# Optimization experiments

Hardware: AMD Instinct MI355X
Metric: run time of the kernel (lower is better)

## Reference

```python
import jax, jax.numpy as jnp
import numpy as np

D_MODEL = 1024
N_HEADS = 16
N_SPECIAL = 4
N_STD = N_HEADS - N_SPECIAL
D_K = D_MODEL // N_HEADS


def setup_inputs() -> dict:
    key = jax.random.key(0)
    ks = jax.random.split(key, 8)
    B, S = 2, 2048
    x = jax.random.normal(ks[0], (B, S, D_MODEL), dtype=jnp.float32)
    input_ids = jax.random.randint(ks[1], (B, S), 0, 32000)
    w = lambda k: jax.random.normal(k, (D_MODEL, D_MODEL), dtype=jnp.float32) * 0.02
    return {
        "x": x,
        "input_ids": input_ids,
        "Wq": w(ks[2]), "bq": jnp.zeros((D_MODEL,), jnp.float32),
        "Wk": w(ks[3]), "bk": jnp.zeros((D_MODEL,), jnp.float32),
        "Wv": w(ks[4]), "bv": jnp.zeros((D_MODEL,), jnp.float32),
        "Wo": w(ks[5]), "bo": jnp.zeros((D_MODEL,), jnp.float32),
    }


def _sdpa(q, k, v):
    # q,k,v: [B, H, S, Dk]
    scale = 1.0 / jnp.sqrt(jnp.float32(D_K))
    scores = jnp.einsum("bhqd,bhkd->bhqk", q, k) * scale
    weights = jax.nn.softmax(scores, axis=-1)
    out = jnp.einsum("bhqk,bhkd->bhqd", weights, v)
    return out, weights


def reference(x, input_ids, Wq, bq, Wk, bk, Wv, bv, Wo, bo):
    B, S, _ = x.shape
    split = lambda t: jnp.transpose(t.reshape(B, S, N_HEADS, D_K), (0, 2, 1, 3))
    q = split(x @ Wq + bq)  # [B, H, S, Dk]
    k = split(x @ Wk + bk)
    v = split(x @ Wv + bv)
    # split head groups: first N_STD standard heads, last N_SPECIAL special heads
    std_out, std_w = _sdpa(q[:, :N_STD], k[:, :N_STD], v[:, :N_STD])
    spec_out, spec_w = _sdpa(q[:, N_STD:], k[:, N_STD:], v[:, N_STD:])
    out = jnp.concatenate([std_out, spec_out], axis=1)  # [B, H, S, Dk]
    out = jnp.transpose(out, (0, 2, 1, 3)).reshape(B, S, D_MODEL)
    out = out @ Wo + bo
    return out, std_w, spec_w
```

## Files before the change

### kernel.cpp

```cpp
#include <hip/hip_runtime.h>
#include <hip/hip_bf16.h>
#include <stdint.h>

#define S_LEN 2048
#define DM    1024
#define NHEAD 16
#define DKH   64

typedef __attribute__((ext_vector_type(8))) short short8;
typedef __attribute__((ext_vector_type(4))) float floatx4;

__device__ __forceinline__ unsigned short f2b(float f) {
  union { float f; unsigned u; } v; v.f = f;
  unsigned u = v.u;
  u += 0x7FFF + ((u >> 16) & 1);
  return (unsigned short)(u >> 16);
}

__global__ void cast_x_kernel(const float* __restrict__ x, unsigned short* __restrict__ xb) {
  int i = (blockIdx.x * 256 + threadIdx.x) * 4;
  float4 v = *(const float4*)(x + i);
  uint2 p;
  p.x = (unsigned)f2b(v.x) | ((unsigned)f2b(v.y) << 16);
  p.y = (unsigned)f2b(v.z) | ((unsigned)f2b(v.w) << 16);
  *(uint2*)(xb + i) = p;
}

__global__ void castT_w_kernel(const float* __restrict__ Wq, const float* __restrict__ Wk,
                               const float* __restrict__ Wv, const float* __restrict__ Wo,
                               unsigned short* __restrict__ Wqt, unsigned short* __restrict__ Wkt,
                               unsigned short* __restrict__ Wvt, unsigned short* __restrict__ Wot) {
  __shared__ __align__(16) unsigned short tile[64][68];
  int z = blockIdx.z;
  const float* W = (z == 0) ? Wq : (z == 1) ? Wk : (z == 2) ? Wv : Wo;
  unsigned short* O = (z == 0) ? Wqt : (z == 1) ? Wkt : (z == 2) ? Wvt : Wot;
  int kbase = blockIdx.y * 64, nbase = blockIdx.x * 64;
  int t = threadIdx.x;
  int r = t >> 4, c = (t & 15) * 4;
#pragma unroll
  for (int i = 0; i < 4; ++i) {
    int row = r + i * 16;
    float4 v = *(const float4*)(W + (size_t)(kbase + row) * DM + nbase + c);
    tile[row][c]     = f2b(v.x); tile[row][c + 1] = f2b(v.y);
    tile[row][c + 2] = f2b(v.z); tile[row][c + 3] = f2b(v.w);
  }
  __syncthreads();
  int n0 = t >> 4, k0 = (t & 15) * 4;
#pragma unroll
  for (int i = 0; i < 4; ++i) {
    int n = n0 + i * 16;
    uint2 p;
    p.x = (unsigned)tile[k0][n]     | ((unsigned)tile[k0 + 1][n] << 16);
    p.y = (unsigned)tile[k0 + 2][n] | ((unsigned)tile[k0 + 3][n] << 16);
    *(uint2*)(O + (size_t)(nbase + n) * DM + kbase + k0) = p;
  }
}

__global__ __launch_bounds__(256) void gemm_kernel(
    const unsigned short* __restrict__ A,
    const unsigned short* __restrict__ Wt0, const unsigned short* __restrict__ Wt1,
    const unsigned short* __restrict__ Wt2,
    const float* __restrict__ b0, const float* __restrict__ b1, const float* __restrict__ b2,
    unsigned short* __restrict__ o0, unsigned short* __restrict__ o1,
    unsigned short* __restrict__ o2, float* __restrict__ o3, int qkv) {
  __shared__ __align__(16) unsigned short sA[128][40];
  __shared__ __align__(16) unsigned short sB[128][40];
  int z = blockIdx.z;
  const unsigned short* Wt = (!qkv || z == 0) ? Wt0 : (z == 1) ? Wt1 : Wt2;
  const float* bias        = (!qkv || z == 0) ? b0  : (z == 1) ? b1  : b2;
  int bm = blockIdx.y, bn = blockIdx.x;
  int t = threadIdx.x;
  int w = t >> 6, lane = t & 63, lm = lane & 15, q4 = lane >> 4;
  int wm = w >> 1, wn = w & 1;
  floatx4 acc[4][4];
#pragma unroll
  for (int i = 0; i < 4; ++i)
#pragma unroll
    for (int j = 0; j < 4; ++j) acc[i][j] = (floatx4){0.f, 0.f, 0.f, 0.f};

  for (int kk = 0; kk < 32; ++kk) {
    __syncthreads();
#pragma unroll
    for (int i = 0; i < 2; ++i) {
      int u = t + 256 * i;
      int row = u >> 2, seg = u & 3;
      *(uint4*)&sA[row][seg * 8] = *(const uint4*)(A + (size_t)(bm * 128 + row) * DM + kk * 32 + seg * 8);
      *(uint4*)&sB[row][seg * 8] = *(const uint4*)(Wt + (size_t)(bn * 128 + row) * DM + kk * 32 + seg * 8);
    }
    __syncthreads();
    short8 af[4], bf[4];
#pragma unroll
    for (int tm = 0; tm < 4; ++tm) af[tm] = *(const short8*)&sA[wm * 64 + tm * 16 + lm][q4 * 8];
#pragma unroll
    for (int tn = 0; tn < 4; ++tn) bf[tn] = *(const short8*)&sB[wn * 64 + tn * 16 + lm][q4 * 8];
#pragma unroll
    for (int tm = 0; tm < 4; ++tm)
#pragma unroll
      for (int tn = 0; tn < 4; ++tn)
        acc[tm][tn] = __builtin_amdgcn_mfma_f32_16x16x32_bf16(af[tm], bf[tn], acc[tm][tn], 0, 0, 0);
  }

  const float qscale = 0.18033688011112042f;
#pragma unroll
  for (int tm = 0; tm < 4; ++tm) {
    int mrow = bm * 128 + wm * 64 + tm * 16 + q4 * 4;
#pragma unroll
    for (int tn = 0; tn < 4; ++tn) {
      int n = bn * 128 + wn * 64 + tn * 16 + lm;
      float bv = bias[n];
#pragma unroll
      for (int r = 0; r < 4; ++r) {
        int m = mrow + r;
        float val = acc[tm][tn][r] + bv;
        if (qkv) {
          int b = m >> 11, s = m & 2047, h = n >> 6, d = n & 63;
          unsigned short* op = (z == 0) ? o0 : (z == 1) ? o1 : o2;
          op[(size_t)((b * NHEAD + h) * S_LEN + s) * DKH + d] = f2b(z == 0 ? val * qscale : val);
        } else {
          o3[(size_t)m * DM + n] = val;
        }
      }
    }
  }
}

__global__ void transpose_v_kernel(const unsigned short* __restrict__ V, unsigned short* __restrict__ Vt) {
  __shared__ __align__(16) unsigned short tile[64][72];
  int b = blockIdx.z, h = blockIdx.y, st = blockIdx.x;
  size_t head = (size_t)(b * NHEAD + h) * S_LEN * DKH;
  int t = threadIdx.x;
#pragma unroll
  for (int i = 0; i < 2; ++i) {
    int u = t + 256 * i;
    int row = u >> 3, seg = u & 7;
    *(uint4*)&tile[row][seg * 8] = *(const uint4*)(V + head + (size_t)(st * 64 + row) * DKH + seg * 8);
  }
  __syncthreads();
#pragma unroll
  for (int i = 0; i < 2; ++i) {
    int u = t + 256 * i;
    int d = u >> 3, sg = u & 7;
    unsigned short vals[8];
#pragma unroll
    for (int j = 0; j < 8; ++j) vals[j] = tile[sg * 8 + j][d];
    uint4 p;
    p.x = (unsigned)vals[0] | ((unsigned)vals[1] << 16);
    p.y = (unsigned)vals[2] | ((unsigned)vals[3] << 16);
    p.z = (unsigned)vals[4] | ((unsigned)vals[5] << 16);
    p.w = (unsigned)vals[6] | ((unsigned)vals[7] << 16);
    *(uint4*)(Vt + head + (size_t)d * S_LEN + st * 64 + sg * 8) = p;
  }
}

__global__ __launch_bounds__(256) void attn_kernel(
    const unsigned short* __restrict__ Q, const unsigned short* __restrict__ K,
    const unsigned short* __restrict__ Vt, float* __restrict__ wout,
    unsigned short* __restrict__ ctx) {
  __shared__ __align__(16) unsigned short sQ[64][72];
  __shared__ __align__(16) unsigned short sK[64][72];
  __shared__ __align__(16) unsigned short sV[64][72];
  __shared__ __align__(16) unsigned short sP[64][72];
  int qt = blockIdx.x, h = blockIdx.y, b = blockIdx.z;
  size_t head = (size_t)(b * NHEAD + h) * S_LEN * DKH;
  int q0 = qt * 64;
  int t = threadIdx.x, w = t >> 6, lane = t & 63, lm = lane & 15, q4 = lane >> 4;
#pragma unroll
  for (int i = 0; i < 2; ++i) {
    int u = t + 256 * i;
    int row = u >> 3, seg = u & 7;
    *(uint4*)&sQ[row][seg * 8] = *(const uint4*)(Q + head + (size_t)(q0 + row) * DKH + seg * 8);
  }
  __syncthreads();
  short8 qf0 = *(const short8*)&sQ[w * 16 + lm][q4 * 8];
  short8 qf1 = *(const short8*)&sQ[w * 16 + lm][32 + q4 * 8];

  float lsum[4] = {0.f, 0.f, 0.f, 0.f};
  for (int c = 0; c < 32; ++c) {
    __syncthreads();
#pragma unroll
    for (int i = 0; i < 2; ++i) {
      int u = t + 256 * i;
      int row = u >> 3, seg = u & 7;
      *(uint4*)&sK[row][seg * 8] = *(const uint4*)(K + head + (size_t)(c * 64 + row) * DKH + seg * 8);
    }
    __syncthreads();
#pragma unroll
    for (int s4 = 0; s4 < 4; ++s4) {
      short8 kf0 = *(const short8*)&sK[s4 * 16 + lm][q4 * 8];
      short8 kf1 = *(const short8*)&sK[s4 * 16 + lm][32 + q4 * 8];
      floatx4 zz = (floatx4){0.f, 0.f, 0.f, 0.f};
      zz = __builtin_amdgcn_mfma_f32_16x16x32_bf16(qf0, kf0, zz, 0, 0, 0);
      zz = __builtin_amdgcn_mfma_f32_16x16x32_bf16(qf1, kf1, zz, 0, 0, 0);
#pragma unroll
      for (int r = 0; r < 4; ++r) lsum[r] += exp2f(zz[r]);
    }
  }
#pragma unroll
  for (int off = 1; off < 16; off <<= 1)
#pragma unroll
    for (int r = 0; r < 4; ++r) lsum[r] += __shfl_xor(lsum[r], off, 64);
  float rl[4];
#pragma unroll
  for (int r = 0; r < 4; ++r) rl[r] = 1.0f / lsum[r];

  size_t wbase = (h < 12) ? (4194304ULL + (size_t)(b * 12 + h) * 4194304ULL)
                          : (104857600ULL + (size_t)(b * 4 + h - 12) * 4194304ULL);

  floatx4 acc[4];
#pragma unroll
  for (int i = 0; i < 4; ++i) acc[i] = (floatx4){0.f, 0.f, 0.f, 0.f};
  for (int c = 0; c < 32; ++c) {
    __syncthreads();
#pragma unroll
    for (int i = 0; i < 2; ++i) {
      int u = t + 256 * i;
      int row = u >> 3, seg = u & 7;
      *(uint4*)&sK[row][seg * 8] = *(const uint4*)(K + head + (size_t)(c * 64 + row) * DKH + seg * 8);
      *(uint4*)&sV[row][seg * 8] = *(const uint4*)(Vt + head + (size_t)row * S_LEN + c * 64 + seg * 8);
    }
    __syncthreads();
#pragma unroll
    for (int s4 = 0; s4 < 4; ++s4) {
      short8 kf0 = *(const short8*)&sK[s4 * 16 + lm][q4 * 8];
      short8 kf1 = *(const short8*)&sK[s4 * 16 + lm][32 + q4 * 8];
      floatx4 zz = (floatx4){0.f, 0.f, 0.f, 0.f};
      zz = __builtin_amdgcn_mfma_f32_16x16x32_bf16(qf0, kf0, zz, 0, 0, 0);
      zz = __builtin_amdgcn_mfma_f32_16x16x32_bf16(qf1, kf1, zz, 0, 0, 0);
#pragma unroll
      for (int r = 0; r < 4; ++r) {
        float p = exp2f(zz[r]) * rl[r];
        wout[wbase + (size_t)(q0 + w * 16 + q4 * 4 + r) * S_LEN + c * 64 + s4 * 16 + lm] = p;
        sP[w * 16 + q4 * 4 + r][s4 * 16 + lm] = f2b(p);
      }
    }
    __syncthreads();
#pragma unroll
    for (int ks = 0; ks < 2; ++ks) {
      short8 pa = *(const short8*)&sP[w * 16 + lm][ks * 32 + q4 * 8];
#pragma unroll
      for (int nt = 0; nt < 4; ++nt) {
        short8 vb = *(const short8*)&sV[nt * 16 + lm][ks * 32 + q4 * 8];
        acc[nt] = __builtin_amdgcn_mfma_f32_16x16x32_bf16(pa, vb, acc[nt], 0, 0, 0);
      }
    }
  }
#pragma unroll
  for (int nt = 0; nt < 4; ++nt)
#pragma unroll
    for (int r = 0; r < 4; ++r)
      ctx[(size_t)(b * S_LEN + q0 + w * 16 + q4 * 4 + r) * DM + h * DKH + nt * 16 + lm] = f2b(acc[nt][r]);
}

extern "C" void kernel_launch(void* const* d_in, const int* in_sizes, int n_in,
                              void* d_out, int out_size, void* d_ws, size_t ws_size,
                              hipStream_t stream) {
  const float* x  = (const float*)d_in[0];
  const float* Wq = (const float*)d_in[2];
  const float* bq = (const float*)d_in[3];
  const float* Wk = (const float*)d_in[4];
  const float* bk = (const float*)d_in[5];
  const float* Wv = (const float*)d_in[6];
  const float* bv = (const float*)d_in[7];
  const float* Wo = (const float*)d_in[8];
  const float* bo = (const float*)d_in[9];
  float* out = (float*)d_out;

  char* ws = (char*)d_ws;
  unsigned short* xb  = (unsigned short*)(ws + 0);
  unsigned short* Wqt = (unsigned short*)(ws + 8388608);
  unsigned short* Wkt = (unsigned short*)(ws + 10485760);
  unsigned short* Wvt = (unsigned short*)(ws + 12582912);
  unsigned short* Wot = (unsigned short*)(ws + 14680064);
  unsigned short* Qb  = (unsigned short*)(ws + 16777216);
  unsigned short* Kb  = (unsigned short*)(ws + 25165824);
  unsigned short* Vb  = (unsigned short*)(ws + 33554432);
  unsigned short* Vtb = (unsigned short*)(ws + 41943040);
  unsigned short* ctx = (unsigned short*)(ws + 50331648);

  cast_x_kernel<<<4096, 256, 0, stream>>>(x, xb);
  castT_w_kernel<<<dim3(16, 16, 4), 256, 0, stream>>>(Wq, Wk, Wv, Wo, Wqt, Wkt, Wvt, Wot);
  gemm_kernel<<<dim3(8, 32, 3), 256, 0, stream>>>(xb, Wqt, Wkt, Wvt, bq, bk, bv,
                                                  Qb, Kb, Vb, nullptr, 1);
  transpose_v_kernel<<<dim3(32, NHEAD, 2), 256, 0, stream>>>(Vb, Vtb);
  attn_kernel<<<dim3(32, NHEAD, 2), 256, 0, stream>>>(Qb, Kb, Vtb, out, ctx);
  gemm_kernel<<<dim3(8, 32, 1), 256, 0, stream>>>(ctx, Wot, nullptr, nullptr, bo, nullptr, nullptr,
                                                  nullptr, nullptr, nullptr, out, 0);
}
```

Before: 816.4 us.

## Transpose QK^T MFMA operands for row-contiguous vectorized weight stores

The K and Q operands of the score MFMA are swapped, so each lane holds four consecutive key columns of a single query row instead of four rows. This makes the row-sum reduction a scalar with two cross-lane shuffles, and lets the fp32 attention-weight output be written as one 16-byte nontemporal store per lane instead of four scattered scalar stores. The bf16 probabilities are packed with a hardware cvt_pk instruction and written to shared memory as one 8-byte store. The main target is the large weights write, which dominates memory traffic. Because the bf16 conversion now uses hardware rounding instead of the software routine, numerics may differ slightly.

```diff
diff --git a/kernel.cpp b/kernel.cpp
--- a/kernel.cpp
+++ b/kernel.cpp
@@ -174,7 +174,7 @@
   short8 qf0 = *(const short8*)&sQ[w * 16 + lm][q4 * 8];
   short8 qf1 = *(const short8*)&sQ[w * 16 + lm][32 + q4 * 8];
 
-  float lsum[4] = {0.f, 0.f, 0.f, 0.f};
+  float lsum = 0.f;
   for (int c = 0; c < 32; ++c) {
     __syncthreads();
 #pragma unroll
@@ -189,22 +189,19 @@
       short8 kf0 = *(const short8*)&sK[s4 * 16 + lm][q4 * 8];
       short8 kf1 = *(const short8*)&sK[s4 * 16 + lm][32 + q4 * 8];
       floatx4 zz = (floatx4){0.f, 0.f, 0.f, 0.f};
-      zz = __builtin_amdgcn_mfma_f32_16x16x32_bf16(qf0, kf0, zz, 0, 0, 0);
-      zz = __builtin_amdgcn_mfma_f32_16x16x32_bf16(qf1, kf1, zz, 0, 0, 0);
-#pragma unroll
-      for (int r = 0; r < 4; ++r) lsum[r] += exp2f(zz[r]);
-    }
-  }
-#pragma unroll
-  for (int off = 1; off < 16; off <<= 1)
-#pragma unroll
-    for (int r = 0; r < 4; ++r) lsum[r] += __shfl_xor(lsum[r], off, 64);
-  float rl[4];
-#pragma unroll
-  for (int r = 0; r < 4; ++r) rl[r] = 1.0f / lsum[r];
+      zz = __builtin_amdgcn_mfma_f32_16x16x32_bf16(kf0, qf0, zz, 0, 0, 0);
+      zz = __builtin_amdgcn_mfma_f32_16x16x32_bf16(kf1, qf1, zz, 0, 0, 0);
+#pragma unroll
+      for (int r = 0; r < 4; ++r) lsum += exp2f(zz[r]);
+    }
+  }
+  lsum += __shfl_xor(lsum, 16, 64);
+  lsum += __shfl_xor(lsum, 32, 64);
+  float rl = 1.0f / lsum;
 
   size_t wbase = (h < 12) ? (4194304ULL + (size_t)(b * 12 + h) * 4194304ULL)
                           : (104857600ULL + (size_t)(b * 4 + h - 12) * 4194304ULL);
+  size_t wrow = wbase + (size_t)(q0 + w * 16 + lm) * S_LEN;
 
   floatx4 acc[4];
 #pragma unroll
@@ -224,14 +221,19 @@
       short8 kf0 = *(const short8*)&sK[s4 * 16 + lm][q4 * 8];
       short8 kf1 = *(const short8*)&sK[s4 * 16 + lm][32 + q4 * 8];
       floatx4 zz = (floatx4){0.f, 0.f, 0.f, 0.f};
-      zz = __builtin_amdgcn_mfma_f32_16x16x32_bf16(qf0, kf0, zz, 0, 0, 0);
-      zz = __builtin_amdgcn_mfma_f32_16x16x32_bf16(qf1, kf1, zz, 0, 0, 0);
-#pragma unroll
-      for (int r = 0; r < 4; ++r) {
-        float p = exp2f(zz[r]) * rl[r];
-        wout[wbase + (size_t)(q0 + w * 16 + q4 * 4 + r) * S_LEN + c * 64 + s4 * 16 + lm] = p;
-        sP[w * 16 + q4 * 4 + r][s4 * 16 + lm] = f2b(p);
-      }
+      zz = __builtin_amdgcn_mfma_f32_16x16x32_bf16(kf0, qf0, zz, 0, 0, 0);
+      zz = __builtin_amdgcn_mfma_f32_16x16x32_bf16(kf1, qf1, zz, 0, 0, 0);
+      float p0 = exp2f(zz[0]) * rl;
+      float p1 = exp2f(zz[1]) * rl;
+      float p2 = exp2f(zz[2]) * rl;
+      float p3 = exp2f(zz[3]) * rl;
+      floatx4 pq = (floatx4){p0, p1, p2, p3};
+      __builtin_nontemporal_store(pq, (floatx4*)(wout + wrow + c * 64 + s4 * 16 + q4 * 4));
+      unsigned pk0, pk1;
+      asm("v_cvt_pk_bf16_f32 %0, %1, %2" : "=v"(pk0) : "v"(p0), "v"(p1));
+      asm("v_cvt_pk_bf16_f32 %0, %1, %2" : "=v"(pk1) : "v"(p2), "v"(p3));
+      uint2 pk; pk.x = pk0; pk.y = pk1;
+      *(uint2*)&sP[w * 16 + lm][s4 * 16 + q4 * 4] = pk;
     }
     __syncthreads();
 #pragma unroll
```

After: 761.0 us. -6.8%, faster.
